# Optimization experiments

Hardware: AMD Instinct MI355X
Metric: run time of the kernel (lower is better)

## Reference

```python
import jax, jax.numpy as jnp
import numpy as np

B, S, D_MODEL, H, DK, DV, DOUT = 8, 2048, 1024, 1, 512, 512, 1024
EPS = 1e-6
TEMP = DK ** 0.5


def _ln(x, g, b):
    # LayerNorm over last dim, eps=1e-6, affine
    m = jnp.mean(x, axis=-1, keepdims=True)
    v = jnp.mean((x - m) ** 2, axis=-1, keepdims=True)
    return (x - m) * jax.lax.rsqrt(v + EPS) * g + b


def setup_inputs() -> dict:
    key = jax.random.key(0)
    ks = jax.random.split(key, 16)
    s = 0.02
    return {
        "q": jax.random.normal(ks[0], (B, S, D_MODEL), jnp.float32),
        "k": jax.random.normal(ks[1], (B, S, D_MODEL), jnp.float32),
        "v": jax.random.normal(ks[2], (B, S, D_MODEL), jnp.float32),
        "mask": jnp.ones((B, S, S), jnp.int32),
        "Wq": jax.random.normal(ks[3], (D_MODEL, H * DK), jnp.float32) * s,
        "bq": jnp.zeros((H * DK,), jnp.float32),
        "Wk": jax.random.normal(ks[4], (D_MODEL, H * DK), jnp.float32) * s,
        "bk": jnp.zeros((H * DK,), jnp.float32),
        "Wv": jax.random.normal(ks[5], (D_MODEL, H * DV), jnp.float32) * s,
        "bv": jnp.zeros((H * DV,), jnp.float32),
        "g_q": jnp.ones((H * DK,), jnp.float32),
        "be_q": jnp.zeros((H * DK,), jnp.float32),
        "g_k": jnp.ones((H * DK,), jnp.float32),
        "be_k": jnp.zeros((H * DK,), jnp.float32),
        "g_v": jnp.ones((H * DV,), jnp.float32),
        "be_v": jnp.zeros((H * DV,), jnp.float32),
        "W1": jax.random.normal(ks[6], (H * DV, H * DV), jnp.float32) * s,
        "b1": jnp.zeros((H * DV,), jnp.float32),
        "W2": jax.random.normal(ks[7], (H * DV, DOUT), jnp.float32) * s,
        "b2": jnp.zeros((DOUT,), jnp.float32),
    }


def reference(q, k, v, mask, Wq, bq, Wk, bk, Wv, bv, g_q, be_q, g_k, be_k, g_v, be_v, W1, b1, W2, b2):
    # QKV projections, viewed as (B, S, H, d)
    qp = (q @ Wq + bq).reshape(B, S, H, DK)
    kp = (k @ Wk + bk).reshape(B, S, H, DK)
    vp = (v @ Wv + bv).reshape(B, S, H, DV)
    residual = qp
    # per-(token,head) LayerNorm over last dim (valid only because H == 1 in source)
    qn = jnp.swapaxes(_ln(qp, g_q, be_q), 1, 2)  # (B, H, S, DK)
    kn = jnp.swapaxes(_ln(kp, g_k, be_k), 1, 2)
    vn = jnp.swapaxes(_ln(vp, g_v, be_v), 1, 2)
    # scaled dot-product attention with mask
    scores = jnp.einsum('bhqd,bhkd->bhqk', qn / TEMP, kn)
    scores = jnp.where(mask[:, None, :, :] == 0, -1e9, scores)
    attn = jax.nn.softmax(scores, axis=-1)
    out = jnp.einsum('bhqk,bhkd->bhqd', attn, vn)
    out = jnp.swapaxes(out, 1, 2).reshape(B, S, H * DV)
    # trailing 2-layer MLP
    out = jax.nn.relu(out @ W1 + b1) @ W2 + b2
    return (out, residual, jnp.squeeze(attn))
```

## Files before the change

kernel.cpp:

```cpp
#include <hip/hip_runtime.h>
#include <hip/hip_bf16.h>

typedef __attribute__((ext_vector_type(8))) short short8;
typedef __attribute__((ext_vector_type(4))) short short4v;
typedef __attribute__((ext_vector_type(4))) float f32x4;

#define INV_TEMP 0.044194173824159216f

__device__ __forceinline__ ushort f2bf(float f) {
  unsigned u = __float_as_uint(f);
  unsigned r = (u + 0x7FFFu + ((u >> 16) & 1u)) >> 16;
  return (ushort)r;
}
__device__ __forceinline__ float bf2f(ushort u) {
  union { unsigned i; float f; } x; x.i = ((unsigned)u) << 16; return x.f;
}

__device__ __forceinline__ void gload_lds16(const void* g, void* l) {
  __builtin_amdgcn_global_load_lds(
      (const __attribute__((address_space(1))) unsigned int*)(unsigned long long)(uintptr_t)g,
      (__attribute__((address_space(3))) unsigned int*)(unsigned)(uintptr_t)l,
      16, 0, 0);
}

__global__ __launch_bounds__(256)
void transpose_cvt_all(const float* __restrict__ Wq, const float* __restrict__ Wk,
                       const float* __restrict__ Wv, const float* __restrict__ W1,
                       const float* __restrict__ W2,
                       ushort* __restrict__ Tq, ushort* __restrict__ Tk,
                       ushort* __restrict__ Tv, ushort* __restrict__ T1,
                       ushort* __restrict__ T2) {
  const int z = blockIdx.z;
  const int K = (z < 3) ? 1024 : 512;
  const int N = (z == 4) ? 1024 : 512;
  if (blockIdx.x * 32 >= N || blockIdx.y * 32 >= K) return;
  const float* W = z == 0 ? Wq : (z == 1 ? Wk : (z == 2 ? Wv : (z == 3 ? W1 : W2)));
  ushort* WT = z == 0 ? Tq : (z == 1 ? Tk : (z == 2 ? Tv : (z == 3 ? T1 : T2)));
  __shared__ float tile[32][33];
  const int n0 = blockIdx.x * 32, k0 = blockIdx.y * 32;
  const int tx = threadIdx.x & 31, ty = threadIdx.x >> 5;
  #pragma unroll
  for (int i = ty; i < 32; i += 8)
    tile[i][tx] = W[(long)(k0 + i) * N + n0 + tx];
  __syncthreads();
  #pragma unroll
  for (int i = ty; i < 32; i += 8)
    WT[(long)(n0 + i) * K + k0 + tx] = f2bf(tile[tx][i]);
}

__global__ __launch_bounds__(256)
void transpose_bf16(const ushort* __restrict__ in, ushort* __restrict__ out, int S, int D) {
  __shared__ ushort tile[32][33];
  const ushort* inb = in + (long)blockIdx.z * S * D;
  ushort* outb = out + (long)blockIdx.z * S * D;
  const int d0 = blockIdx.x * 32, s0 = blockIdx.y * 32;
  const int tx = threadIdx.x & 31, ty = threadIdx.x >> 5;
  #pragma unroll
  for (int i = ty; i < 32; i += 8)
    tile[i][tx] = inb[(long)(s0 + i) * D + d0 + tx];
  __syncthreads();
  #pragma unroll
  for (int i = ty; i < 32; i += 8)
    outb[(long)(d0 + i) * S + s0 + tx] = tile[tx][i];
}

__global__ __launch_bounds__(256)
void ln3_kernel(const float* __restrict__ Xq, const ushort* __restrict__ Xk,
                const ushort* __restrict__ Xv,
                const float* __restrict__ gq, const float* __restrict__ beq,
                const float* __restrict__ gk, const float* __restrict__ bek,
                const float* __restrict__ gv, const float* __restrict__ bev,
                ushort* __restrict__ Oq, ushort* __restrict__ Ok, ushort* __restrict__ Ov) {
  const int which = blockIdx.y;
  const float* g = which == 0 ? gq : (which == 1 ? gk : gv);
  const float* be = which == 0 ? beq : (which == 1 ? bek : bev);
  ushort* out = which == 0 ? Oq : (which == 1 ? Ok : Ov);
  const float scale = which == 0 ? INV_TEMP : 1.0f;

  const int row = blockIdx.x * 4 + (threadIdx.x >> 6);
  const int lane = threadIdx.x & 63;
  f32x4 v0, v1;
  if (which == 0) {
    const float* x = Xq + (long)row * 512 + lane * 8;
    v0 = *(const f32x4*)x;
    v1 = *(const f32x4*)(x + 4);
  } else {
    const ushort* x = (which == 1 ? Xk : Xv) + (long)row * 512 + lane * 8;
    short8 vv = *(const short8*)x;
    #pragma unroll
    for (int j = 0; j < 4; j++) { v0[j] = bf2f((ushort)vv[j]); v1[j] = bf2f((ushort)vv[4 + j]); }
  }
  float s = v0[0]+v0[1]+v0[2]+v0[3]+v1[0]+v1[1]+v1[2]+v1[3];
  float ss = v0[0]*v0[0]+v0[1]*v0[1]+v0[2]*v0[2]+v0[3]*v0[3]
           + v1[0]*v1[0]+v1[1]*v1[1]+v1[2]*v1[2]+v1[3]*v1[3];
  #pragma unroll
  for (int off = 32; off; off >>= 1) { s += __shfl_xor(s, off); ss += __shfl_xor(ss, off); }
  const float mean = s * (1.0f/512.0f);
  const float var  = ss * (1.0f/512.0f) - mean*mean;
  const float rs = rsqrtf(var + 1e-6f);
  f32x4 g0 = *(const f32x4*)(g + lane*8);
  f32x4 g1 = *(const f32x4*)(g + lane*8 + 4);
  f32x4 b0 = *(const f32x4*)(be + lane*8);
  f32x4 b1 = *(const f32x4*)(be + lane*8 + 4);
  union { short8 v; ushort u[8]; } o;
  #pragma unroll
  for (int j = 0; j < 4; j++) o.u[j]     = f2bf(((v0[j]-mean)*rs*g0[j] + b0[j]) * scale);
  #pragma unroll
  for (int j = 0; j < 4; j++) o.u[4 + j] = f2bf(((v1[j]-mean)*rs*g1[j] + b1[j]) * scale);
  *(short8*)(out + (long)row * 512 + lane * 8) = o.v;
}

__global__ __launch_bounds__(256)
void invz_reduce(const float* __restrict__ partial, float* __restrict__ invZ) {
  const int r = blockIdx.x * 256 + threadIdx.x;
  const int zb = r >> 11, s = r & 2047;
  float z = 0.f;
  #pragma unroll
  for (int j = 0; j < 16; j++) z += partial[((zb * 16 + j) << 11) + s];
  invZ[r] = 1.0f / z;
}

template<int EPI, bool HAS_BIAS, bool OUT_BF16, bool A_F32>
__global__ __launch_bounds__(256)
void gemm_tn(const void* __restrict__ Av, const ushort* __restrict__ Bt,
             const float* __restrict__ bias, const int* __restrict__ mask,
             float* __restrict__ Cf, ushort* __restrict__ Cb,
             float* __restrict__ partial, const float* __restrict__ invZ,
             int M, int N, int K,
             long sA, long sB, long sC, long sMask) {
  __shared__ ushort As[128 * 64];
  __shared__ ushort Bs[128 * 64];
  __shared__ float zloc[128];
  const int tid = threadIdx.x;
  const int lane = tid & 63;
  const int wave = tid >> 6;
  const int wr = wave >> 1, wc = wave & 1;

  const int gx = gridDim.x, gy = gridDim.y;
  int lin = blockIdx.x + gx * (blockIdx.y + gy * blockIdx.z);
  const int nwg = gx * gy * (int)gridDim.z;
  int swz = lin;
  if ((nwg & 7) == 0) {
    const int q8 = nwg >> 3;
    swz = (lin & 7) * q8 + (lin >> 3);
  }
  const int bx = swz % gx;
  const int tmp = swz / gx;
  const int by = tmp % gy;
  const int bz = tmp / gy;

  const long zb = bz;
  const ushort* Ab = (const ushort*)Av + zb * sA + (long)by * 128 * K;
  const float*  Af = (const float*)Av + zb * sA + (long)by * 128 * K;
  const ushort* Bb = Bt + zb * sB + (long)bx * 128 * K;
  const int rowbase0 = by * 128;

  if constexpr (EPI == 3) {
    if (tid < 128) zloc[tid] = invZ[zb * 2048 + rowbase0 + tid];
  }

  f32x4 acc[4][4];
  #pragma unroll
  for (int m = 0; m < 4; m++)
    #pragma unroll
    for (int n = 0; n < 4; n++)
      acc[m][n] = f32x4{0.f, 0.f, 0.f, 0.f};

  for (int kt = 0; kt < K; kt += 64) {
    #pragma unroll
    for (int i = 0; i < 4; i++) {
      const int c = i * 256 + tid;
      const int row = c >> 3;
      const int g = c & 7;
      const int gsrc = g ^ (row & 7);
      gload_lds16(Bb + (long)row * K + kt + gsrc * 8, (char*)Bs + c * 16);
      if constexpr (A_F32) {
        const f32x4 u0 = *(const f32x4*)(Af + (long)row * K + kt + g * 8);
        const f32x4 u1 = *(const f32x4*)(Af + (long)row * K + kt + g * 8 + 4);
        union { short8 s; ushort u[8]; } o;
        #pragma unroll
        for (int j = 0; j < 4; j++) { o.u[j] = f2bf(u0[j]); o.u[4 + j] = f2bf(u1[j]); }
        *(short8*)((char*)As + ((row << 7) | ((g << 4) ^ ((row & 7) << 4)))) = o.s;
      } else {
        gload_lds16(Ab + (long)row * K + kt + gsrc * 8, (char*)As + c * 16);
      }
    }
    __syncthreads();

    if constexpr (EPI == 3) {
      if (bx == 0) {
        #pragma unroll
        for (int i = 0; i < 4; i++) {
          const int c = i * 256 + tid;
          const int row = c >> 3;
          const int j = c & 7;
          short8 p8 = *(const short8*)((const char*)As + ((row << 7) | ((j ^ (row & 7)) << 4)));
          const float iz = zloc[row];
          f32x4 o0, o1;
          #pragma unroll
          for (int jj = 0; jj < 4; jj++) {
            o0[jj] = bf2f((ushort)p8[jj]) * iz;
            o1[jj] = bf2f((ushort)p8[4 + jj]) * iz;
          }
          float* dst = Cf + zb * 4194304L + (long)(rowbase0 + row) * 2048 + kt + j * 8;
          *(f32x4*)dst = o0;
          *(f32x4*)(dst + 4) = o1;
        }
      }
    }

    #pragma unroll
    for (int ks = 0; ks < 2; ks++) {
      short8 af[4], bfr[4];
      const int kb = ks * 64 + ((lane >> 4) << 4);
      #pragma unroll
      for (int m = 0; m < 4; m++) {
        const int row = wr * 64 + m * 16 + (lane & 15);
        af[m] = *(const short8*)((const char*)As + ((row << 7) | (kb ^ ((row & 7) << 4))));
      }
      #pragma unroll
      for (int n = 0; n < 4; n++) {
        const int col = wc * 64 + n * 16 + (lane & 15);
        bfr[n] = *(const short8*)((const char*)Bs + ((col << 7) | (kb ^ ((col & 7) << 4))));
      }
      #pragma unroll
      for (int m = 0; m < 4; m++)
        #pragma unroll
        for (int n = 0; n < 4; n++)
          acc[m][n] = __builtin_amdgcn_mfma_f32_16x16x32_bf16(af[m], bfr[n], acc[m][n], 0, 0, 0);
    }
    __syncthreads();
  }

  const int colbase = bx * 128 + wc * 64;
  const int rowbase = by * 128 + wr * 64;
  const int c_lane = lane & 15;
  const int r_lane = (lane >> 4) << 2;

  float rs_acc[4][4];
  if constexpr (EPI == 2) {
    #pragma unroll
    for (int m = 0; m < 4; m++)
      #pragma unroll
      for (int r4 = 0; r4 < 4; r4++) rs_acc[m][r4] = 0.f;
  }

  #pragma unroll
  for (int n = 0; n < 4; n++) {
    const int col = colbase + n * 16 + c_lane;
    const float bv = HAS_BIAS ? bias[col] : 0.0f;
    #pragma unroll
    for (int m = 0; m < 4; m++) {
      const int rbase = rowbase + m * 16 + r_lane;
      #pragma unroll
      for (int r4 = 0; r4 < 4; r4++) {
        const int row = rbase + r4;
        float vv = acc[m][n][r4] + bv;
        if constexpr (EPI == 1) vv = fmaxf(vv, 0.0f);
        if constexpr (EPI == 2) {
          const int mk = mask[zb * sMask + (long)row * N + col];
          vv = mk ? __expf(vv) : 0.0f;
          rs_acc[m][r4] += vv;
        }
        if constexpr (EPI == 3) vv *= zloc[wr * 64 + m * 16 + r_lane + r4];
        const long off = zb * sC + (long)row * N + col;
        if constexpr (OUT_BF16) Cb[off] = f2bf(vv);
        else                    Cf[off] = vv;
      }
    }
  }

  if constexpr (EPI == 2) {
    float (*red)[128] = (float(*)[128])As;
    #pragma unroll
    for (int m = 0; m < 4; m++)
      #pragma unroll
      for (int r4 = 0; r4 < 4; r4++) {
        float vsum = rs_acc[m][r4];
        vsum += __shfl_xor(vsum, 1);
        vsum += __shfl_xor(vsum, 2);
        vsum += __shfl_xor(vsum, 4);
        vsum += __shfl_xor(vsum, 8);
        if (c_lane == 0) red[wc][wr * 64 + m * 16 + r_lane + r4] = vsum;
      }
    __syncthreads();
    if (tid < 128)
      partial[((long)zb * 16 + bx) * 2048 + by * 128 + tid] = red[0][tid] + red[1][tid];
  }
}

extern "C" void kernel_launch(void* const* d_in, const int* in_sizes, int n_in,
                              void* d_out, int out_size, void* d_ws, size_t ws_size,
                              hipStream_t stream) {
  const float* q    = (const float*)d_in[0];
  const float* k    = (const float*)d_in[1];
  const float* v    = (const float*)d_in[2];
  const int*   mask = (const int*)d_in[3];
  const float* Wq   = (const float*)d_in[4];
  const float* bq   = (const float*)d_in[5];
  const float* Wk   = (const float*)d_in[6];
  const float* bk   = (const float*)d_in[7];
  const float* Wv   = (const float*)d_in[8];
  const float* bv   = (const float*)d_in[9];
  const float* g_q  = (const float*)d_in[10];
  const float* be_q = (const float*)d_in[11];
  const float* g_k  = (const float*)d_in[12];
  const float* be_k = (const float*)d_in[13];
  const float* g_v  = (const float*)d_in[14];
  const float* be_v = (const float*)d_in[15];
  const float* W1   = (const float*)d_in[16];
  const float* b1   = (const float*)d_in[17];
  const float* W2   = (const float*)d_in[18];
  const float* b2   = (const float*)d_in[19];

  float* out_mlp  = (float*)d_out;
  float* out_res  = out_mlp + 16777216L;
  float* out_attn = out_res + 8388608L;

  char* w = (char*)d_ws;
  ushort* qn      = (ushort*)(w);
  ushort* kn      = (ushort*)(w + 16777216UL);
  ushort* kp_bf   = (ushort*)(w + 33554432UL);
  ushort* vp_bf   = (ushort*)(w + 50331648UL);
  ushort* attn_bf = (ushort*)(w + 33554432UL);
  ushort* vn      = (ushort*)(w + 100663296UL);
  ushort* vnT     = (ushort*)(w + 117440512UL);
  ushort* pv      = (ushort*)(w + 134217728UL);
  ushort* h       = (ushort*)(w + 150994944UL);
  ushort* wqT     = (ushort*)(w + 167772160UL);
  ushort* wkT     = (ushort*)(w + 168820736UL);
  ushort* wvT     = (ushort*)(w + 169869312UL);
  ushort* w1T     = (ushort*)(w + 170917888UL);
  ushort* w2T     = (ushort*)(w + 171442176UL);
  float*  partial = (float*)(w + 172490752UL);
  float*  invZ    = (float*)(w + 173539328UL);

  dim3 blk(256);

  transpose_cvt_all<<<dim3(32, 32, 5), blk, 0, stream>>>(
      Wq, Wk, Wv, W1, W2, wqT, wkT, wvT, w1T, w2T);

  gemm_tn<0, true, false, true><<<dim3(4, 128, 1), blk, 0, stream>>>(
      q, wqT, bq, nullptr, out_res, nullptr, nullptr, nullptr,
      16384, 512, 1024, 0, 0, 0, 0);
  gemm_tn<0, true, true, true><<<dim3(4, 128, 1), blk, 0, stream>>>(
      k, wkT, bk, nullptr, nullptr, kp_bf, nullptr, nullptr,
      16384, 512, 1024, 0, 0, 0, 0);
  gemm_tn<0, true, true, true><<<dim3(4, 128, 1), blk, 0, stream>>>(
      v, wvT, bv, nullptr, nullptr, vp_bf, nullptr, nullptr,
      16384, 512, 1024, 0, 0, 0, 0);

  ln3_kernel<<<dim3(4096, 3), blk, 0, stream>>>(
      out_res, kp_bf, vp_bf, g_q, be_q, g_k, be_k, g_v, be_v, qn, kn, vn);

  transpose_bf16<<<dim3(16, 64, 8), blk, 0, stream>>>(vn, vnT, 2048, 512);

  gemm_tn<2, false, true, false><<<dim3(16, 16, 8), blk, 0, stream>>>(
      qn, kn, nullptr, mask, nullptr, attn_bf, partial, nullptr,
      2048, 2048, 512,
      (long)2048 * 512, (long)2048 * 512, (long)2048 * 2048, (long)2048 * 2048);

  invz_reduce<<<64, blk, 0, stream>>>(partial, invZ);

  gemm_tn<3, false, true, false><<<dim3(4, 16, 8), blk, 0, stream>>>(
      attn_bf, vnT, nullptr, nullptr, out_attn, pv, nullptr, invZ,
      2048, 512, 2048,
      (long)2048 * 2048, (long)512 * 2048, (long)2048 * 512, 0);

  gemm_tn<1, true, true, false><<<dim3(4, 128, 1), blk, 0, stream>>>(
      pv, w1T, b1, nullptr, nullptr, h, nullptr, nullptr,
      16384, 512, 512, 0, 0, 0, 0);
  gemm_tn<0, true, false, false><<<dim3(8, 128, 1), blk, 0, stream>>>(
      h, w2T, b2, nullptr, out_mlp, nullptr, nullptr, nullptr,
      16384, 1024, 512, 0, 0, 0, 0);
}
```

Before: 421.8 us.

## Double-buffer GEMM LDS tiles with 512-thread blocks and spread attn write

Replaces the single-buffered 256-thread GEMM with a double-buffered variant that prefetches two k-tiles ahead, using explicit vmcnt waits and raw s_barrier so global loads overlap MFMA work. Blocks grow to 8 waves (2x4), each computing 64x32 instead of 64x64, and the EPI==2 row-sum reduction now combines four column partials. The normalized attention output write in the PV GEMM is spread across all bx blocks by k-tile instead of falling entirely on bx==0. Doubled LDS (about 64KB) and more waves per block may limit occupancy, and the hand-written waitcnt counts are fragile.

```diff
diff --git a/kernel.cpp b/kernel.cpp
--- a/kernel.cpp
+++ b/kernel.cpp
@@ -121,20 +121,21 @@
 }
 
 template<int EPI, bool HAS_BIAS, bool OUT_BF16, bool A_F32>
-__global__ __launch_bounds__(256)
-void gemm_tn(const void* __restrict__ Av, const ushort* __restrict__ Bt,
-             const float* __restrict__ bias, const int* __restrict__ mask,
-             float* __restrict__ Cf, ushort* __restrict__ Cb,
-             float* __restrict__ partial, const float* __restrict__ invZ,
-             int M, int N, int K,
-             long sA, long sB, long sC, long sMask) {
-  __shared__ ushort As[128 * 64];
-  __shared__ ushort Bs[128 * 64];
+__global__ __launch_bounds__(512)
+void gemm_tn_pipe(const void* __restrict__ Av, const ushort* __restrict__ Bt,
+                  const float* __restrict__ bias, const int* __restrict__ mask,
+                  float* __restrict__ Cf, ushort* __restrict__ Cb,
+                  float* __restrict__ partial, const float* __restrict__ invZ,
+                  int M, int N, int K,
+                  long sA, long sB, long sC, long sMask) {
+  __shared__ ushort As[2][128 * 64];
+  __shared__ ushort Bs[2][128 * 64];
   __shared__ float zloc[128];
   const int tid = threadIdx.x;
   const int lane = tid & 63;
   const int wave = tid >> 6;
-  const int wr = wave >> 1, wc = wave & 1;
+  const int wr = wave >> 2;
+  const int wc = wave & 3;
 
   const int gx = gridDim.x, gy = gridDim.y;
   int lin = blockIdx.x + gx * (blockIdx.y + gy * blockIdx.z);
@@ -154,47 +155,78 @@
   const float*  Af = (const float*)Av + zb * sA + (long)by * 128 * K;
   const ushort* Bb = Bt + zb * sB + (long)bx * 128 * K;
   const int rowbase0 = by * 128;
+  const int nt = K >> 6;
 
   if constexpr (EPI == 3) {
     if (tid < 128) zloc[tid] = invZ[zb * 2048 + rowbase0 + tid];
   }
 
-  f32x4 acc[4][4];
+  auto stage = [&](int buf, int t) {
+    const long kt = (long)t << 6;
+    if constexpr (A_F32) {
+      const int c0 = tid, c1 = 512 + tid;
+      const float* p0 = Af + (long)(c0 >> 3) * K + kt + (c0 & 7) * 8;
+      const float* p1 = Af + (long)(c1 >> 3) * K + kt + (c1 & 7) * 8;
+      f32x4 a00 = *(const f32x4*)p0;
+      f32x4 a01 = *(const f32x4*)(p0 + 4);
+      f32x4 a10 = *(const f32x4*)p1;
+      f32x4 a11 = *(const f32x4*)(p1 + 4);
+      #pragma unroll
+      for (int e = 0; e < 2; e++) {
+        const int c = e * 512 + tid;
+        const int row = c >> 3, g = c & 7, gsrc = g ^ (row & 7);
+        gload_lds16(Bb + (long)row * K + kt + gsrc * 8, (char*)Bs[buf] + c * 16);
+      }
+      union { short8 s; ushort u[8]; } o0, o1;
+      #pragma unroll
+      for (int j = 0; j < 4; j++) {
+        o0.u[j] = f2bf(a00[j]); o0.u[4 + j] = f2bf(a01[j]);
+        o1.u[j] = f2bf(a10[j]); o1.u[4 + j] = f2bf(a11[j]);
+      }
+      const int r0 = c0 >> 3, g0 = c0 & 7, r1 = c1 >> 3, g1 = c1 & 7;
+      *(short8*)((char*)As[buf] + ((r0 << 7) | ((g0 << 4) ^ ((r0 & 7) << 4)))) = o0.s;
+      *(short8*)((char*)As[buf] + ((r1 << 7) | ((g1 << 4) ^ ((r1 & 7) << 4)))) = o1.s;
+    } else {
+      #pragma unroll
+      for (int e = 0; e < 2; e++) {
+        const int c = e * 512 + tid;
+        const int row = c >> 3, g = c & 7, gsrc = g ^ (row & 7);
+        gload_lds16(Ab + (long)row * K + kt + gsrc * 8, (char*)As[buf] + c * 16);
+        gload_lds16(Bb + (long)row * K + kt + gsrc * 8, (char*)Bs[buf] + c * 16);
+      }
+    }
+  };
+
+  f32x4 acc[4][2];
   #pragma unroll
   for (int m = 0; m < 4; m++)
     #pragma unroll
-    for (int n = 0; n < 4; n++)
+    for (int n = 0; n < 2; n++)
       acc[m][n] = f32x4{0.f, 0.f, 0.f, 0.f};
 
-  for (int kt = 0; kt < K; kt += 64) {
-    #pragma unroll
-    for (int i = 0; i < 4; i++) {
-      const int c = i * 256 + tid;
-      const int row = c >> 3;
-      const int g = c & 7;
-      const int gsrc = g ^ (row & 7);
-      gload_lds16(Bb + (long)row * K + kt + gsrc * 8, (char*)Bs + c * 16);
-      if constexpr (A_F32) {
-        const f32x4 u0 = *(const f32x4*)(Af + (long)row * K + kt + g * 8);
-        const f32x4 u1 = *(const f32x4*)(Af + (long)row * K + kt + g * 8 + 4);
-        union { short8 s; ushort u[8]; } o;
+  stage(0, 0);
+  stage(1, 1);
+
+  for (int t = 0; t < nt; ++t) {
+    const int buf = t & 1;
+    if (t == nt - 1) {
+      asm volatile("s_waitcnt vmcnt(0)" ::: "memory");
+    } else if constexpr (A_F32) {
+      asm volatile("s_waitcnt vmcnt(2)" ::: "memory");
+    } else {
+      asm volatile("s_waitcnt vmcnt(4)" ::: "memory");
+    }
+    __builtin_amdgcn_s_barrier();
+    __builtin_amdgcn_sched_barrier(0);
+
+    if constexpr (EPI == 3) {
+      if ((t >> 3) == bx) {
         #pragma unroll
-        for (int j = 0; j < 4; j++) { o.u[j] = f2bf(u0[j]); o.u[4 + j] = f2bf(u1[j]); }
-        *(short8*)((char*)As + ((row << 7) | ((g << 4) ^ ((row & 7) << 4)))) = o.s;
-      } else {
-        gload_lds16(Ab + (long)row * K + kt + gsrc * 8, (char*)As + c * 16);
-      }
-    }
-    __syncthreads();
-
-    if constexpr (EPI == 3) {
-      if (bx == 0) {
-        #pragma unroll
-        for (int i = 0; i < 4; i++) {
-          const int c = i * 256 + tid;
-          const int row = c >> 3;
-          const int j = c & 7;
-          short8 p8 = *(const short8*)((const char*)As + ((row << 7) | ((j ^ (row & 7)) << 4)));
+        for (int e = 0; e < 2; e++) {
+          const int c = e * 512 + tid;
+          const int row = c >> 3, g = c & 7;
+          short8 p8 = *(const short8*)((const char*)As[buf] +
+                       ((row << 7) | ((g ^ (row & 7)) << 4)));
           const float iz = zloc[row];
           f32x4 o0, o1;
           #pragma unroll
@@ -202,7 +234,7 @@
             o0[jj] = bf2f((ushort)p8[jj]) * iz;
             o1[jj] = bf2f((ushort)p8[4 + jj]) * iz;
           }
-          float* dst = Cf + zb * 4194304L + (long)(rowbase0 + row) * 2048 + kt + j * 8;
+          float* dst = Cf + zb * 4194304L + (long)(rowbase0 + row) * 2048 + (t << 6) + g * 8;
           *(f32x4*)dst = o0;
           *(f32x4*)(dst + 4) = o1;
         }
@@ -211,28 +243,33 @@
 
     #pragma unroll
     for (int ks = 0; ks < 2; ks++) {
-      short8 af[4], bfr[4];
+      short8 af[4], bfr[2];
       const int kb = ks * 64 + ((lane >> 4) << 4);
       #pragma unroll
       for (int m = 0; m < 4; m++) {
         const int row = wr * 64 + m * 16 + (lane & 15);
-        af[m] = *(const short8*)((const char*)As + ((row << 7) | (kb ^ ((row & 7) << 4))));
-      }
-      #pragma unroll
-      for (int n = 0; n < 4; n++) {
-        const int col = wc * 64 + n * 16 + (lane & 15);
-        bfr[n] = *(const short8*)((const char*)Bs + ((col << 7) | (kb ^ ((col & 7) << 4))));
+        af[m] = *(const short8*)((const char*)As[buf] +
+                 ((row << 7) | (kb ^ ((row & 7) << 4))));
+      }
+      #pragma unroll
+      for (int n = 0; n < 2; n++) {
+        const int col = wc * 32 + n * 16 + (lane & 15);
+        bfr[n] = *(const short8*)((const char*)Bs[buf] +
+                  ((col << 7) | (kb ^ ((col & 7) << 4))));
       }
       #pragma unroll
       for (int m = 0; m < 4; m++)
         #pragma unroll
-        for (int n = 0; n < 4; n++)
+        for (int n = 0; n < 2; n++)
           acc[m][n] = __builtin_amdgcn_mfma_f32_16x16x32_bf16(af[m], bfr[n], acc[m][n], 0, 0, 0);
     }
-    __syncthreads();
-  }
-
-  const int colbase = bx * 128 + wc * 64;
+    __builtin_amdgcn_sched_barrier(0);
+    __builtin_amdgcn_s_barrier();
+    __builtin_amdgcn_sched_barrier(0);
+    if (t + 2 < nt) stage(buf, t + 2);
+  }
+
+  const int colbase = bx * 128 + wc * 32;
   const int rowbase = by * 128 + wr * 64;
   const int c_lane = lane & 15;
   const int r_lane = (lane >> 4) << 2;
@@ -246,7 +283,7 @@
   }
 
   #pragma unroll
-  for (int n = 0; n < 4; n++) {
+  for (int n = 0; n < 2; n++) {
     const int col = colbase + n * 16 + c_lane;
     const float bv = HAS_BIAS ? bias[col] : 0.0f;
     #pragma unroll
@@ -271,6 +308,7 @@
   }
 
   if constexpr (EPI == 2) {
+    __syncthreads();
     float (*red)[128] = (float(*)[128])As;
     #pragma unroll
     for (int m = 0; m < 4; m++)
@@ -285,7 +323,8 @@
       }
     __syncthreads();
     if (tid < 128)
-      partial[((long)zb * 16 + bx) * 2048 + by * 128 + tid] = red[0][tid] + red[1][tid];
+      partial[((long)zb * 16 + bx) * 2048 + by * 128 + tid] =
+          red[0][tid] + red[1][tid] + red[2][tid] + red[3][tid];
   }
 }
 
@@ -336,17 +375,18 @@
   float*  invZ    = (float*)(w + 173539328UL);
 
   dim3 blk(256);
+  dim3 blk512(512);
 
   transpose_cvt_all<<<dim3(32, 32, 5), blk, 0, stream>>>(
       Wq, Wk, Wv, W1, W2, wqT, wkT, wvT, w1T, w2T);
 
-  gemm_tn<0, true, false, true><<<dim3(4, 128, 1), blk, 0, stream>>>(
+  gemm_tn_pipe<0, true, false, true><<<dim3(4, 128, 1), blk512, 0, stream>>>(
       q, wqT, bq, nullptr, out_res, nullptr, nullptr, nullptr,
       16384, 512, 1024, 0, 0, 0, 0);
-  gemm_tn<0, true, true, true><<<dim3(4, 128, 1), blk, 0, stream>>>(
+  gemm_tn_pipe<0, true, true, true><<<dim3(4, 128, 1), blk512, 0, stream>>>(
       k, wkT, bk, nullptr, nullptr, kp_bf, nullptr, nullptr,
       16384, 512, 1024, 0, 0, 0, 0);
-  gemm_tn<0, true, true, true><<<dim3(4, 128, 1), blk, 0, stream>>>(
+  gemm_tn_pipe<0, true, true, true><<<dim3(4, 128, 1), blk512, 0, stream>>>(
       v, wvT, bv, nullptr, nullptr, vp_bf, nullptr, nullptr,
       16384, 512, 1024, 0, 0, 0, 0);
 
@@ -355,22 +395,22 @@
 
   transpose_bf16<<<dim3(16, 64, 8), blk, 0, stream>>>(vn, vnT, 2048, 512);
 
-  gemm_tn<2, false, true, false><<<dim3(16, 16, 8), blk, 0, stream>>>(
+  gemm_tn_pipe<2, false, true, false><<<dim3(16, 16, 8), blk512, 0, stream>>>(
       qn, kn, nullptr, mask, nullptr, attn_bf, partial, nullptr,
       2048, 2048, 512,
       (long)2048 * 512, (long)2048 * 512, (long)2048 * 2048, (long)2048 * 2048);
 
   invz_reduce<<<64, blk, 0, stream>>>(partial, invZ);
 
-  gemm_tn<3, false, true, false><<<dim3(4, 16, 8), blk, 0, stream>>>(
+  gemm_tn_pipe<3, false, true, false><<<dim3(4, 16, 8), blk512, 0, stream>>>(
       attn_bf, vnT, nullptr, nullptr, out_attn, pv, nullptr, invZ,
       2048, 512, 2048,
       (long)2048 * 2048, (long)512 * 2048, (long)2048 * 512, 0);
 
-  gemm_tn<1, true, true, false><<<dim3(4, 128, 1), blk, 0, stream>>>(
+  gemm_tn_pipe<1, true, true, false><<<dim3(4, 128, 1), blk512, 0, stream>>>(
       pv, w1T, b1, nullptr, nullptr, h, nullptr, nullptr,
       16384, 512, 512, 0, 0, 0, 0);
-  gemm_tn<0, true, false, false><<<dim3(8, 128, 1), blk, 0, stream>>>(
+  gemm_tn_pipe<0, true, false, false><<<dim3(8, 128, 1), blk512, 0, stream>>>(
       h, w2T, b2, nullptr, out_mlp, nullptr, nullptr, nullptr,
       16384, 1024, 512, 0, 0, 0, 0);
 }
```

Measured after the change: 376.5 us. 1.12x faster.
